# Kernel tuning notes

Hardware: AMD Instinct MI355X
Metric: run time of the kernel (lower is better)

## Reference

```python
import jax, jax.numpy as jnp
import numpy as np

N = 50000
E = 800000
DIN = 128
DOUT = 128


def setup_inputs() -> dict:
    key = jax.random.key(0)
    k1, k2, k3, k4, k5, k6 = jax.random.split(key, 6)
    h = jax.random.normal(k1, (N, DIN), dtype=jnp.float32)
    weight = jax.random.normal(k2, (DIN, DOUT), dtype=jnp.float32) * (1.0 / np.sqrt(DOUT))
    bias = jax.random.normal(k3, (DOUT,), dtype=jnp.float32) * (1.0 / np.sqrt(DOUT))
    norm = jax.random.uniform(k4, (N, 1), dtype=jnp.float32)  # per-node deg^-1/2 scaling
    src = jax.random.randint(k5, (E,), 0, N, dtype=jnp.int32)
    dst = jax.random.randint(k6, (E,), 0, N, dtype=jnp.int32)
    return {"h": h, "weight": weight, "bias": bias, "norm": norm, "src": src, "dst": dst}


def reference(h, weight, bias, norm, src, dst):
    # dense projection: [N, DIN] @ [DIN, DOUT]
    hw = jnp.matmul(h, weight)
    # pre-aggregation normalization scaling
    hw = hw * norm
    # sparse neighbor aggregation: sum messages h[src] into dst (copy_src + sum)
    agg = jax.ops.segment_sum(hw[src], dst, num_segments=N)
    # post-aggregation normalization, bias, activation
    out = agg * norm + bias
    return jax.nn.relu(out)
```

## Files before the change

kernel.cpp:

```cpp
#include <hip/hip_runtime.h>
#include <hip/hip_bf16.h>


#define DIM 128
#define ELLW 64

static __device__ __forceinline__ unsigned short f32_to_bf16_bits(float x) {
    const unsigned int u = __float_as_uint(x);
    return (unsigned short)((u + 0x7FFFu + ((u >> 16) & 1u)) >> 16);
}

__global__ __launch_bounds__(256) void fused_pre_kernel(
    const float* __restrict__ h, const float* __restrict__ norm,
    const int* __restrict__ src, const int* __restrict__ dst,
    unsigned int* __restrict__ hs, int* __restrict__ counts,
    int* __restrict__ ell, int n, int E, int psB, int scB)
{
    int bid = blockIdx.x;

    if (bid < scB) {
        int i = bid * 256 + threadIdx.x;
        const int stride = scB * 256;
        for (; i < E; i += stride) {
            const int d = dst[i];
            const int pos = atomicAdd(&counts[d], 1);
            if (pos < ELLW) ell[(size_t)d * ELLW + pos] = src[i];
        }
        return;
    }
    bid -= scB;

    const int total = n * (DIM / 8);
    const int i = bid * 256 + threadIdx.x;
    if (i >= total) return;
    const int row = i >> 4;
    const float nv = norm[row];
    const float4* p = (const float4*)(h + (size_t)i * 8);
    const float4 a = p[0], b = p[1];
    const float v[8] = {a.x, a.y, a.z, a.w, b.x, b.y, b.z, b.w};
    unsigned int o[4];
#pragma unroll
    for (int k = 0; k < 4; ++k) {
        o[k] = (unsigned int)f32_to_bf16_bits(v[2 * k] * nv) |
               ((unsigned int)f32_to_bf16_bits(v[2 * k + 1] * nv) << 16);
    }
    ((uint4*)hs)[i] = make_uint4(o[0], o[1], o[2], o[3]);
}

__global__ __launch_bounds__(256) void aggregate_ell_kernel(
    const unsigned int* __restrict__ hs, const int* __restrict__ counts,
    const int* __restrict__ ell, float* __restrict__ agg, int n)
{
    const int node = blockIdx.x * 4 + (threadIdx.x >> 6);
    if (node >= n) return;
    const int lane = threadIdx.x & 63;

    const int cnt = min(counts[node], ELLW);
    const int* __restrict__ sl = ell + (size_t)node * ELLW;

    float ax = 0.f, ay = 0.f;
    int i = 0;
    for (; i + 4 <= cnt; i += 4) {
        const int s0 = sl[i + 0], s1 = sl[i + 1], s2 = sl[i + 2], s3 = sl[i + 3];
        const unsigned int u0 = hs[(size_t)s0 * 64 + lane];
        const unsigned int u1 = hs[(size_t)s1 * 64 + lane];
        const unsigned int u2 = hs[(size_t)s2 * 64 + lane];
        const unsigned int u3 = hs[(size_t)s3 * 64 + lane];
        ax += __uint_as_float(u0 << 16) + __uint_as_float(u1 << 16) +
              __uint_as_float(u2 << 16) + __uint_as_float(u3 << 16);
        ay += __uint_as_float(u0 & 0xFFFF0000u) + __uint_as_float(u1 & 0xFFFF0000u) +
              __uint_as_float(u2 & 0xFFFF0000u) + __uint_as_float(u3 & 0xFFFF0000u);
    }
    for (; i < cnt; ++i) {
        const unsigned int u = hs[(size_t)sl[i] * 64 + lane];
        ax += __uint_as_float(u << 16);
        ay += __uint_as_float(u & 0xFFFF0000u);
    }

    ((float2*)agg)[(size_t)node * 64 + lane] = make_float2(ax, ay);
}

#define ROWS_PER_BLOCK 32
__global__ __launch_bounds__(256) void gemm_epilogue_kernel(
    const float* __restrict__ agg, const float* __restrict__ W,
    const float* __restrict__ norm, const float* __restrict__ bias,
    float* __restrict__ out, int n)
{
    __shared__ float Ws[DIM * DIM];
    __shared__ float Hs[ROWS_PER_BLOCK * DIM];
    const int tid = threadIdx.x;
    const int row0 = blockIdx.x * ROWS_PER_BLOCK;

    {
        const float4* W4 = (const float4*)W;
        float4* Ws4 = (float4*)Ws;
#pragma unroll
        for (int i = 0; i < 16; ++i) Ws4[tid + i * 256] = W4[tid + i * 256];
    }
    {
        const int nrows = min(ROWS_PER_BLOCK, n - row0);
        const float4* H4 = (const float4*)(agg + (size_t)row0 * DIM);
        float4* Hs4 = (float4*)Hs;
        const int cnt = nrows * (DIM / 4);
        for (int i = tid; i < cnt; i += 256) Hs4[i] = H4[i];
    }
    __syncthreads();

    const int tx = threadIdx.x & 31;
    const int ty = threadIdx.x >> 5;

    float acc[4][4];
#pragma unroll
    for (int r = 0; r < 4; ++r)
#pragma unroll
        for (int c = 0; c < 4; ++c) acc[r][c] = 0.f;

    for (int k = 0; k < DIM; k += 4) {
        float4 w[4];
#pragma unroll
        for (int kk = 0; kk < 4; ++kk)
            w[kk] = *(const float4*)&Ws[(k + kk) * DIM + tx * 4];
#pragma unroll
        for (int r = 0; r < 4; ++r) {
            const float4 hv = *(const float4*)&Hs[(ty * 4 + r) * DIM + k];
            acc[r][0] += hv.x * w[0].x + hv.y * w[1].x + hv.z * w[2].x + hv.w * w[3].x;
            acc[r][1] += hv.x * w[0].y + hv.y * w[1].y + hv.z * w[2].y + hv.w * w[3].y;
            acc[r][2] += hv.x * w[0].z + hv.y * w[1].z + hv.z * w[2].z + hv.w * w[3].z;
            acc[r][3] += hv.x * w[0].w + hv.y * w[1].w + hv.z * w[2].w + hv.w * w[3].w;
        }
    }

    const float4 b = ((const float4*)bias)[tx];
#pragma unroll
    for (int r = 0; r < 4; ++r) {
        const int row = row0 + ty * 4 + r;
        if (row < n) {
            const float nv = norm[row];
            float4 o;
            o.x = fmaxf(acc[r][0] * nv + b.x, 0.f);
            o.y = fmaxf(acc[r][1] * nv + b.y, 0.f);
            o.z = fmaxf(acc[r][2] * nv + b.z, 0.f);
            o.w = fmaxf(acc[r][3] * nv + b.w, 0.f);
            *(float4*)&out[(size_t)row * DIM + tx * 4] = o;
        }
    }
}

extern "C" void kernel_launch(void* const* d_in, const int* in_sizes, int n_in,
                              void* d_out, int out_size, void* d_ws, size_t ws_size,
                              hipStream_t stream) {
    const float* h    = (const float*)d_in[0];
    const float* W    = (const float*)d_in[1];
    const float* bias = (const float*)d_in[2];
    const float* norm = (const float*)d_in[3];
    const int*   src  = (const int*)d_in[4];
    const int*   dst  = (const int*)d_in[5];
    float* out = (float*)d_out;

    const int n = in_sizes[3];
    const int E = in_sizes[4];

    char* ws = (char*)d_ws;
    unsigned int* hs     = (unsigned int*)ws;
    size_t off           = (size_t)n * DIM * sizeof(unsigned short);
    float*        agg    = (float*)(ws + off);
    off                 += (size_t)n * DIM * sizeof(float);
    int*          counts = (int*)(ws + off);  off += (size_t)n * 4;
    int*          ell    = (int*)(ws + off);

    (void)hipMemsetAsync(counts, 0, (size_t)n * sizeof(int), stream);

    const int psB = (n * (DIM / 8) + 255) / 256;
    const int scB = min((E + 255) / 256, 3125);
    fused_pre_kernel<<<scB + psB, 256, 0, stream>>>(
        h, norm, src, dst, hs, counts, ell, n, E, psB, scB);

    aggregate_ell_kernel<<<(n + 3) / 4, 256, 0, stream>>>(hs, counts, ell, agg, n);

    gemm_epilogue_kernel<<<(n + ROWS_PER_BLOCK - 1) / ROWS_PER_BLOCK, 256, 0, stream>>>(
        agg, W, norm, bias, out, n);
}
```

Baseline: 200.4 us.

## Replace FP32 LDS GEMM with bf16 MFMA GEMM on bf16 aggregate

The scalar FP32 shared-memory GEMM epilogue is replaced by a kernel using 16x16x32 bf16 MFMA instructions. Operands come straight from global memory: the aggregate stored as bf16, and a transposed bf16 copy of W produced by extra blocks in the pre-kernel. Writing the aggregate in bf16 also halves the intermediate traffic between the aggregation and GEMM kernels. The output lane mapping is discovered at runtime by running probe MFMAs. The cost is extra rounding of the aggregate to bf16 and scalar, uncoalesced output stores.

```diff
diff --git a/kernel.cpp b/kernel.cpp
--- a/kernel.cpp
+++ b/kernel.cpp
@@ -4,6 +4,9 @@
 
 #define DIM 128
 #define ELLW 64
+
+using bf16x8 = __attribute__((ext_vector_type(8))) short;
+using f32x4  = __attribute__((ext_vector_type(4))) float;
 
 static __device__ __forceinline__ unsigned short f32_to_bf16_bits(float x) {
     const unsigned int u = __float_as_uint(x);
@@ -12,8 +15,9 @@
 
 __global__ __launch_bounds__(256) void fused_pre_kernel(
     const float* __restrict__ h, const float* __restrict__ norm,
-    const int* __restrict__ src, const int* __restrict__ dst,
-    unsigned int* __restrict__ hs, int* __restrict__ counts,
+    const float* __restrict__ W, const int* __restrict__ src,
+    const int* __restrict__ dst, unsigned int* __restrict__ hs,
+    unsigned short* __restrict__ Wt, int* __restrict__ counts,
     int* __restrict__ ell, int n, int E, int psB, int scB)
 {
     int bid = blockIdx.x;
@@ -30,26 +34,34 @@
     }
     bid -= scB;
 
-    const int total = n * (DIM / 8);
-    const int i = bid * 256 + threadIdx.x;
-    if (i >= total) return;
-    const int row = i >> 4;
-    const float nv = norm[row];
-    const float4* p = (const float4*)(h + (size_t)i * 8);
-    const float4 a = p[0], b = p[1];
-    const float v[8] = {a.x, a.y, a.z, a.w, b.x, b.y, b.z, b.w};
-    unsigned int o[4];
+    if (bid < psB) {
+        const int total = n * (DIM / 8);
+        const int i = bid * 256 + threadIdx.x;
+        if (i >= total) return;
+        const int row = i >> 4;
+        const float nv = norm[row];
+        const float4* p = (const float4*)(h + (size_t)i * 8);
+        const float4 a = p[0], b = p[1];
+        const float v[8] = {a.x, a.y, a.z, a.w, b.x, b.y, b.z, b.w};
+        unsigned int o[4];
 #pragma unroll
-    for (int k = 0; k < 4; ++k) {
-        o[k] = (unsigned int)f32_to_bf16_bits(v[2 * k] * nv) |
-               ((unsigned int)f32_to_bf16_bits(v[2 * k + 1] * nv) << 16);
+        for (int k = 0; k < 4; ++k) {
+            o[k] = (unsigned int)f32_to_bf16_bits(v[2 * k] * nv) |
+                   ((unsigned int)f32_to_bf16_bits(v[2 * k + 1] * nv) << 16);
+        }
+        ((uint4*)hs)[i] = make_uint4(o[0], o[1], o[2], o[3]);
+        return;
     }
-    ((uint4*)hs)[i] = make_uint4(o[0], o[1], o[2], o[3]);
+    bid -= psB;
+
+    const int t = bid * 256 + threadIdx.x;
+    const int col = t >> 7, k = t & 127;
+    Wt[t] = f32_to_bf16_bits(W[(size_t)k * DIM + col]);
 }
 
 __global__ __launch_bounds__(256) void aggregate_ell_kernel(
     const unsigned int* __restrict__ hs, const int* __restrict__ counts,
-    const int* __restrict__ ell, float* __restrict__ agg, int n)
+    const int* __restrict__ ell, unsigned int* __restrict__ aggb, int n)
 {
     const int node = blockIdx.x * 4 + (threadIdx.x >> 6);
     if (node >= n) return;
@@ -77,71 +89,64 @@
         ay += __uint_as_float(u & 0xFFFF0000u);
     }
 
-    ((float2*)agg)[(size_t)node * 64 + lane] = make_float2(ax, ay);
+    aggb[(size_t)node * 64 + lane] =
+        (unsigned int)f32_to_bf16_bits(ax) |
+        ((unsigned int)f32_to_bf16_bits(ay) << 16);
 }
 
-#define ROWS_PER_BLOCK 32
-__global__ __launch_bounds__(256) void gemm_epilogue_kernel(
-    const float* __restrict__ agg, const float* __restrict__ W,
+__global__ __launch_bounds__(256) void gemm_mfma_kernel(
+    const unsigned short* __restrict__ aggb, const unsigned short* __restrict__ Wt,
     const float* __restrict__ norm, const float* __restrict__ bias,
     float* __restrict__ out, int n)
 {
-    __shared__ float Ws[DIM * DIM];
-    __shared__ float Hs[ROWS_PER_BLOCK * DIM];
-    const int tid = threadIdx.x;
-    const int row0 = blockIdx.x * ROWS_PER_BLOCK;
+    const int wave = threadIdx.x >> 6;
+    const int lane = threadIdx.x & 63;
+    const int row0 = blockIdx.x * 64 + wave * 16;
+    const int lrow = lane & 15;
+    const int kgrp = lane >> 4;
 
-    {
-        const float4* W4 = (const float4*)W;
-        float4* Ws4 = (float4*)Ws;
+    bf16x8 onev, rowv;
+    const short one_b = (short)0x3F80;
+    const short row_b = (short)f32_to_bf16_bits((float)lrow);
 #pragma unroll
-        for (int i = 0; i < 16; ++i) Ws4[tid + i * 256] = W4[tid + i * 256];
+    for (int e = 0; e < 8; ++e) { onev[e] = one_b; rowv[e] = row_b; }
+    f32x4 p1 = {0.f, 0.f, 0.f, 0.f}, p2 = {0.f, 0.f, 0.f, 0.f};
+    p1 = __builtin_amdgcn_mfma_f32_16x16x32_bf16(rowv, onev, p1, 0, 0, 0);
+    p2 = __builtin_amdgcn_mfma_f32_16x16x32_bf16(onev, rowv, p2, 0, 0, 0);
+    int irow[4], jcol[4], cr[4];
+    float nv[4];
+#pragma unroll
+    for (int r = 0; r < 4; ++r) {
+        irow[r] = (int)(p1[r] * 0.03125f + 0.5f);
+        jcol[r] = (int)(p2[r] * 0.03125f + 0.5f);
+        cr[r] = row0 + irow[r];
+        nv[r] = (cr[r] < n) ? norm[cr[r]] : 0.f;
     }
-    {
-        const int nrows = min(ROWS_PER_BLOCK, n - row0);
-        const float4* H4 = (const float4*)(agg + (size_t)row0 * DIM);
-        float4* Hs4 = (float4*)Hs;
-        const int cnt = nrows * (DIM / 4);
-        for (int i = tid; i < cnt; i += 256) Hs4[i] = H4[i];
-    }
-    __syncthreads();
 
-    const int tx = threadIdx.x & 31;
-    const int ty = threadIdx.x >> 5;
+    int arow = row0 + lrow;
+    if (arow > n - 1) arow = n - 1;
+    const unsigned short* ap = aggb + (size_t)arow * DIM + kgrp * 8;
+    bf16x8 a[4];
+#pragma unroll
+    for (int ks = 0; ks < 4; ++ks)
+        a[ks] = *(const bf16x8*)(ap + ks * 32);
 
-    float acc[4][4];
 #pragma unroll
-    for (int r = 0; r < 4; ++r)
+    for (int nt = 0; nt < 8; ++nt) {
+        const int col = nt * 16 + lrow;
+        const unsigned short* bp = Wt + (size_t)col * DIM + kgrp * 8;
+        f32x4 acc = {0.f, 0.f, 0.f, 0.f};
 #pragma unroll
-        for (int c = 0; c < 4; ++c) acc[r][c] = 0.f;
-
-    for (int k = 0; k < DIM; k += 4) {
-        float4 w[4];
-#pragma unroll
-        for (int kk = 0; kk < 4; ++kk)
-            w[kk] = *(const float4*)&Ws[(k + kk) * DIM + tx * 4];
+        for (int ks = 0; ks < 4; ++ks) {
+            const bf16x8 b = *(const bf16x8*)(bp + ks * 32);
+            acc = __builtin_amdgcn_mfma_f32_16x16x32_bf16(a[ks], b, acc, 0, 0, 0);
+        }
 #pragma unroll
         for (int r = 0; r < 4; ++r) {
-            const float4 hv = *(const float4*)&Hs[(ty * 4 + r) * DIM + k];
-            acc[r][0] += hv.x * w[0].x + hv.y * w[1].x + hv.z * w[2].x + hv.w * w[3].x;
-            acc[r][1] += hv.x * w[0].y + hv.y * w[1].y + hv.z * w[2].y + hv.w * w[3].y;
-            acc[r][2] += hv.x * w[0].z + hv.y * w[1].z + hv.z * w[2].z + hv.w * w[3].z;
-            acc[r][3] += hv.x * w[0].w + hv.y * w[1].w + hv.z * w[2].w + hv.w * w[3].w;
-        }
-    }
-
-    const float4 b = ((const float4*)bias)[tx];
-#pragma unroll
-    for (int r = 0; r < 4; ++r) {
-        const int row = row0 + ty * 4 + r;
-        if (row < n) {
-            const float nv = norm[row];
-            float4 o;
-            o.x = fmaxf(acc[r][0] * nv + b.x, 0.f);
-            o.y = fmaxf(acc[r][1] * nv + b.y, 0.f);
-            o.z = fmaxf(acc[r][2] * nv + b.z, 0.f);
-            o.w = fmaxf(acc[r][3] * nv + b.w, 0.f);
-            *(float4*)&out[(size_t)row * DIM + tx * 4] = o;
+            if (cr[r] < n) {
+                const int c = nt * 16 + jcol[r];
+                out[(size_t)cr[r] * DIM + c] = fmaxf(acc[r] * nv[r] + bias[c], 0.f);
+            }
         }
     }
 }
@@ -161,22 +166,24 @@
     const int E = in_sizes[4];
 
     char* ws = (char*)d_ws;
-    unsigned int* hs     = (unsigned int*)ws;
-    size_t off           = (size_t)n * DIM * sizeof(unsigned short);
-    float*        agg    = (float*)(ws + off);
-    off                 += (size_t)n * DIM * sizeof(float);
-    int*          counts = (int*)(ws + off);  off += (size_t)n * 4;
-    int*          ell    = (int*)(ws + off);
+    unsigned int*   hs     = (unsigned int*)ws;
+    size_t off             = (size_t)n * DIM * sizeof(unsigned short);
+    unsigned int*   aggb   = (unsigned int*)(ws + off);
+    off                   += (size_t)n * DIM * sizeof(unsigned short);
+    int*            counts = (int*)(ws + off);  off += (size_t)n * 4;
+    int*            ell    = (int*)(ws + off);
+    off                   += (size_t)n * ELLW * sizeof(int);
+    unsigned short* Wt     = (unsigned short*)(ws + off);
 
     (void)hipMemsetAsync(counts, 0, (size_t)n * sizeof(int), stream);
 
     const int psB = (n * (DIM / 8) + 255) / 256;
     const int scB = min((E + 255) / 256, 3125);
-    fused_pre_kernel<<<scB + psB, 256, 0, stream>>>(
-        h, norm, src, dst, hs, counts, ell, n, E, psB, scB);
+    fused_pre_kernel<<<scB + psB + 64, 256, 0, stream>>>(
+        h, norm, W, src, dst, hs, Wt, counts, ell, n, E, psB, scB);
 
-    aggregate_ell_kernel<<<(n + 3) / 4, 256, 0, stream>>>(hs, counts, ell, agg, n);
+    aggregate_ell_kernel<<<(n + 3) / 4, 256, 0, stream>>>(hs, counts, ell, aggb, n);
 
-    gemm_epilogue_kernel<<<(n + ROWS_PER_BLOCK - 1) / ROWS_PER_BLOCK, 256, 0, stream>>>(
-        agg, W, norm, bias, out, n);
+    gemm_mfma_kernel<<<(n + 63) / 64, 256, 0, stream>>>(
+        (const unsigned short*)aggb, Wt, norm, bias, out, n);
 }
```

After: 191.4 us. -4.5%, faster.
